# Performance work log

Measured on AMD Instinct MI355X. Metric: run time of the kernel, lower is better.

## Reference

```python
import jax, jax.numpy as jnp
import numpy as np

HS = WS = 1024      # downsampled mask dims (8192 / scale_factor 8)
K = 24              # kernel_num
KD = 35             # kernel_dim1 == kernel_dim2
OFF = HS // 2 - KD // 2  # offset_s = 495
MASK_STEEP = 4.0
MASK_SHIFT = 0.5
RESIST_STEEP = 50.0
RESIST_TH = 0.225
MAX_DOSE = 1.02
MIN_DOSE = 0.98
POOL = 3            # avepool_kernel


def setup_inputs() -> dict:
    key = jax.random.key(0)
    ks = jax.random.split(key, 7)
    return {
        "mask_s": jax.random.uniform(ks[0], (1, 1, HS, WS), dtype=jnp.float32),
        "kf_re": jax.random.normal(ks[1], (K, KD, KD), dtype=jnp.float32),
        "kf_im": jax.random.normal(ks[2], (K, KD, KD), dtype=jnp.float32),
        "kd_re": jax.random.normal(ks[3], (K, KD, KD), dtype=jnp.float32),
        "kd_im": jax.random.normal(ks[4], (K, KD, KD), dtype=jnp.float32),
        "kf_scale": jax.random.uniform(ks[5], (K, 1, 1), dtype=jnp.float32),
        "kd_scale": jax.random.uniform(ks[6], (K, 1, 1), dtype=jnp.float32),
    }


def _avgpool3(x):
    # AvgPool2d(kernel=3, stride=1, pad=1), count_include_pad=True -> always /9
    s = jax.lax.reduce_window(x, 0.0, jax.lax.add, (1, 1, POOL, POOL),
                              (1, 1, 1, 1),
                              [(0, 0), (0, 0), (POOL // 2, POOL // 2), (POOL // 2, POOL // 2)])
    return s / float(POOL * POOL)


def _dose_branch(crop, kernel, scale, dose):
    # crop: [1,1,KD,KD] complex ; kernel: [K,KD,KD] complex ; scale: [K,1,1]
    buf = jnp.zeros((1, K, HS, WS), dtype=jnp.complex64)
    buf = buf.at[:, :, OFF:OFF + KD, OFF:OFF + KD].set(crop * dose * kernel)
    img = jnp.fft.ifft2(buf)                      # [1,K,HS,WS] complex
    inten = (img.real * img.real + img.imag * img.imag) * scale
    inten = jnp.sum(inten, axis=1, keepdims=True)  # [1,1,HS,WS]
    return jax.nn.sigmoid(RESIST_STEEP * (inten - RESIST_TH))


def reference(mask_s, kf_re, kf_im, kd_re, kd_im, kf_scale, kd_scale):
    kf = jax.lax.complex(kf_re, kf_im)
    kd = jax.lax.complex(kd_re, kd_im)
    mask = jax.nn.sigmoid(MASK_STEEP * (_avgpool3(mask_s) - MASK_SHIFT))
    mf = jnp.fft.fftshift(jnp.fft.fft2(mask), axes=(-2, -1))  # [1,1,HS,WS]
    crop = mf[:, :, OFF:OFF + KD, OFF:OFF + KD]               # [1,1,KD,KD]
    x_nom = _dose_branch(crop, kf, kf_scale, 1.0)
    x_max = _dose_branch(crop, kf, kf_scale, MAX_DOSE)
    x_min = _dose_branch(crop, kd, kd_scale, MIN_DOSE)
    return x_nom, x_max, x_min
```

## Files before the change

### kernel.cpp

```cpp
#include <hip/hip_runtime.h>
#include <math.h>

#define HS 1024
#define WS 1024
#define KK 24
#define KD 35
#define NF 35
#define NDP 69
#define NTUP (2*KK*NDP)
#define CROW 40
#define PROW 37

#define G_OFF    0u
#define CROP_OFF 286720u
#define D_OFF    296520u
#define ZERO_QWORDS 6055

__global__ __launch_bounds__(256) void k_maskG(const float* __restrict__ ms,
                                               float2* __restrict__ G,
                                               unsigned long long* __restrict__ zq) {
    __shared__ float cs[WS + 2];
    __shared__ float m[WS];
    __shared__ float2 part[252];
    const int x = blockIdx.x;
    const int t = threadIdx.x;

    if (x < 24) {
        int i = x * 256 + t;
        if (i < ZERO_QWORDS) zq[i] = 0ull;
    }
    for (int j = t; j < WS; j += 256) {
        float a = (x > 0)      ? ms[(x - 1) * WS + j] : 0.0f;
        float b =                ms[x * WS + j];
        float d = (x < HS - 1) ? ms[(x + 1) * WS + j] : 0.0f;
        cs[j + 1] = a + b + d;
    }
    if (t == 0) { cs[0] = 0.0f; cs[WS + 1] = 0.0f; }
    __syncthreads();
    for (int j = t; j < WS; j += 256) {
        float pool = (cs[j] + cs[j + 1] + cs[j + 2]) * (1.0f / 9.0f);
        m[j] = 1.0f / (1.0f + expf(-4.0f * (pool - 0.5f)));
    }
    __syncthreads();
    if (t < 252) {
        const int qi = t / 14, seg = t % 14;
        float si, ci, ss, cc;
        sincospif(-(float)(qi * seg) * (1.0f / 512.0f), &si, &ci);
        sincospif(-(float)(qi * 14)  * (1.0f / 512.0f), &ss, &cc);
        float wr = ci, wi = si;
        float re = 0.0f, im = 0.0f;
        for (int y = seg; y < WS; y += 14) {
            float mv = m[y];
            re += mv * wr;
            im += mv * wi;
            float nr = wr * cc - wi * ss;
            wi = wr * ss + wi * cc;
            wr = nr;
        }
        part[t] = make_float2(re, im);
    }
    __syncthreads();
    if (t < 18) {
        float re = 0.0f, im = 0.0f;
        for (int s = 0; s < 14; ++s) { float2 p = part[t * 14 + s]; re += p.x; im += p.y; }
        G[(17 + t) * HS + x] = make_float2(re, im);
        if (t > 0) G[(17 - t) * HS + x] = make_float2(re, -im);
    }
}

__global__ __launch_bounds__(256) void k_crop(const float2* __restrict__ G,
                                              float2* __restrict__ crop) {
    __shared__ float2 g2[128];
    __shared__ float2 part[245];
    const int q  = blockIdx.x >> 3;
    const int xs = (blockIdx.x & 7) * 128;
    const int t  = threadIdx.x;
    if (t < 128) g2[t] = G[q * HS + xs + t];
    __syncthreads();
    if (t < 245) {
        const int p = t / 7, seg = t % 7;
        const int v = p - 17;
        float si, ci, ss, cc;
        sincospif((float)(v * (xs + seg)) * (1.0f / 512.0f), &si, &ci);
        sincospif((float)(v * 7)          * (1.0f / 512.0f), &ss, &cc);
        float wr = ci, wi = si;
        float re = 0.0f, im = 0.0f;
        for (int r = seg; r < 128; r += 7) {
            float2 gv = g2[r];
            re += gv.x * wr + gv.y * wi;
            im += gv.y * wr - gv.x * wi;
            float nr = wr * cc - wi * ss;
            wi = wr * ss + wi * cc;
            wr = nr;
        }
        part[t] = make_float2(re, im);
    }
    __syncthreads();
    if (t < NF) {
        float re = 0.0f, im = 0.0f;
        for (int s = 0; s < 7; ++s) { float2 p2 = part[t * 7 + s]; re += p2.x; im += p2.y; }
        float* dst = (float*)&crop[t * NF + q];
        atomicAdd(dst,     re);
        atomicAdd(dst + 1, im);
    }
}

__global__ __launch_bounds__(256) void k_D(
    const float2* __restrict__ crop,
    const float* __restrict__ kre0, const float* __restrict__ kim0,
    const float* __restrict__ kre1, const float* __restrict__ kim1,
    const float* __restrict__ sc0,  const float* __restrict__ sc1,
    float2* __restrict__ D)
{
    __shared__ float2 C[KD * CROW];
    __shared__ float2 partR[28 * PROW];
    const int tup = blockIdx.x;
    const int t   = threadIdx.x;

    const int b   = tup / (KK * NDP);
    const int rem = tup % (KK * NDP);
    const int k   = rem / NDP;
    const int idp = rem % NDP;
    const int dp  = idp - 34;
    const float* kre = b ? kre1 : kre0;
    const float* kim = b ? kim1 : kim0;
    const float dosefac = (b ? 0.98f : 1.0f) * (1.0f / 1048576.0f);
    const float sk2 = ((b ? sc1 : sc0)[k]) * dosefac * dosefac;

    if (t < 175) C[(t / 5) * CROW + 35 + (t % 5)] = make_float2(0.0f, 0.0f);
    #pragma unroll
    for (int j = 0; j < 5; ++j) {
        int i = t + j * 256;
        if (i < KD * KD) {
            float2 c = crop[i];
            int row = i / 35, col = i % 35;
            float kr = kre[k * KD * KD + i], ki = kim[k * KD * KD + i];
            C[row * CROW + col] = make_float2(c.x * kr - c.y * ki,
                                              c.x * ki + c.y * kr);
        }
    }
    __syncthreads();
    if (t < 252) {
        const int tile = t / 28;
        const int r    = t % 28;
        const int pgrp = r / 7;
        const int seg  = r % 7;
        const int d0   = tile * 4;
        const int plo = max(0, dp), phi = min(34, 34 + dp);
        float2 ac0 = {0,0}, ac1 = {0,0}, ac2 = {0,0}, ac3 = {0,0};
        for (int p = plo + pgrp; p <= phi; p += 4) {
            const float2* rowa = &C[p * CROW + d0];
            const float2* rowb = &C[(p - dp) * CROW];
            for (int u = seg; u <= 34 - d0; u += 7) {
                float2 bb = rowb[u];
                float2 a0 = rowa[u], a1 = rowa[u + 1], a2 = rowa[u + 2], a3 = rowa[u + 3];
                ac0.x += a0.x * bb.x + a0.y * bb.y;  ac0.y += a0.y * bb.x - a0.x * bb.y;
                ac1.x += a1.x * bb.x + a1.y * bb.y;  ac1.y += a1.y * bb.x - a1.x * bb.y;
                ac2.x += a2.x * bb.x + a2.y * bb.y;  ac2.y += a2.y * bb.x - a2.x * bb.y;
                ac3.x += a3.x * bb.x + a3.y * bb.y;  ac3.y += a3.y * bb.x - a3.x * bb.y;
            }
        }
        const int base = r * PROW + tile * 4;
        partR[base]     = ac0;
        partR[base + 1] = ac1;
        partR[base + 2] = ac2;
        partR[base + 3] = ac3;
    }
    __syncthreads();
    if (t < NF) {
        float re = 0.0f, im = 0.0f;
        for (int r = 0; r < 28; ++r) {
            float2 v = partR[r * PROW + t];
            re += v.x; im += v.y;
        }
        float* dst = (float*)&D[(b * NDP + idp) * NF + t];
        atomicAdd(dst,     re * sk2);
        atomicAdd(dst + 1, im * sk2);
    }
}

__global__ __launch_bounds__(256) void k_final(const float2* __restrict__ D,
                                               float* __restrict__ out) {
    __shared__ float2 partB[210];
    __shared__ float2 B[2][NF];
    const int x = blockIdx.x;
    const int t = threadIdx.x;
    if (t < 210) {
        const int s = t / 70, r = t % 70, b = r / 35, dq = r % 35;
        float si, ci, ss, cc;
        sincospif((float)((23 * s - 34) * x) * (1.0f / 512.0f), &si, &ci);
        sincospif((float)x                   * (1.0f / 512.0f), &ss, &cc);
        float wr = ci, wi = si;
        float re = 0.0f, im = 0.0f;
        const int i0 = 23 * s;
        for (int idp = i0; idp < i0 + 23; ++idp) {
            float2 d = D[(b * NDP + idp) * NF + dq];
            re += d.x * wr - d.y * wi;
            im += d.x * wi + d.y * wr;
            float nr = wr * cc - wi * ss;
            wi = wr * ss + wi * cc;
            wr = nr;
        }
        partB[t] = make_float2(re, im);
    }
    __syncthreads();
    if (t < 70) {
        float2 a = partB[t], b2 = partB[t + 70], c = partB[t + 140];
        B[t / 35][t % 35] = make_float2(a.x + b2.x + c.x, a.y + b2.y + c.y);
    }
    __syncthreads();
    const float bf0 = B[0][0].x;
    const float bd0 = B[1][0].x;
    for (int y = t; y < WS; y += 256) {
        float s1, c1;
        sincospif((float)y * (1.0f / 512.0f), &s1, &c1);
        float curx = c1, cury = s1;
        float sf = 0.0f, sd = 0.0f;
        #pragma unroll
        for (int dq = 1; dq < NF; ++dq) {
            float2 bf = B[0][dq], bd2 = B[1][dq];
            sf += bf.x * curx - bf.y * cury;
            sd += bd2.x * curx - bd2.y * cury;
            float nx = curx * c1 - cury * s1;
            cury = curx * s1 + cury * c1;
            curx = nx;
        }
        float If = bf0 + 2.0f * sf;
        float Id = bd0 + 2.0f * sd;
        int o = x * WS + y;
        out[o]               = 1.0f / (1.0f + expf(-50.0f * (If - 0.225f)));
        out[o + HS * WS]     = 1.0f / (1.0f + expf(-50.0f * (1.0404f * If - 0.225f)));
        out[o + 2 * HS * WS] = 1.0f / (1.0f + expf(-50.0f * (Id - 0.225f)));
    }
}

extern "C" void kernel_launch(void* const* d_in, const int* in_sizes, int n_in,
                              void* d_out, int out_size, void* d_ws, size_t ws_size,
                              hipStream_t stream) {
    (void)in_sizes; (void)n_in; (void)out_size; (void)ws_size;
    const float* ms    = (const float*)d_in[0];
    const float* kf_re = (const float*)d_in[1];
    const float* kf_im = (const float*)d_in[2];
    const float* kd_re = (const float*)d_in[3];
    const float* kd_im = (const float*)d_in[4];
    const float* kf_sc = (const float*)d_in[5];
    const float* kd_sc = (const float*)d_in[6];

    char* ws = (char*)d_ws;
    float2* G      = (float2*)(ws + G_OFF);
    float2* crop   = (float2*)(ws + CROP_OFF);
    float2* D      = (float2*)(ws + D_OFF);
    unsigned long long* zq = (unsigned long long*)(ws + CROP_OFF);
    float* out     = (float*)d_out;

    k_maskG<<<HS, 256, 0, stream>>>(ms, G, zq);
    k_crop<<<NF * 8, 256, 0, stream>>>(G, crop);
    k_D<<<NTUP, 256, 0, stream>>>(crop, kf_re, kf_im, kd_re, kd_im, kf_sc, kd_sc, D);
    k_final<<<HS, 256, 0, stream>>>(D, out);
}
```

Measured before the change: 58.76 us.

## Vectorize pooling loads, register-tile correlation inner loop, and write outputs as float4

The mask pooling stage now has each thread load and store four contiguous floats with float4 accesses instead of strided scalar loops. The correlation kernel gives each thread a contiguous 5-element u segment, which it unrolls with a sliding register window so A loads are reused, and the C row pad grows to 42. The final output stage computes four adjacent columns per thread and stores float4 vectors to all three outputs. The aim is fewer memory transactions and LDS loads, at the cost of more live registers per thread.

Result: slower. 61.61 us (+4.9%).

```diff
diff --git a/kernel.cpp b/kernel.cpp
--- a/kernel.cpp
+++ b/kernel.cpp
@@ -8,7 +8,7 @@
 #define NF 35
 #define NDP 69
 #define NTUP (2*KK*NDP)
-#define CROW 40
+#define CROW 42
 #define PROW 37
 
 #define G_OFF    0u
@@ -19,7 +19,7 @@
 __global__ __launch_bounds__(256) void k_maskG(const float* __restrict__ ms,
                                                float2* __restrict__ G,
                                                unsigned long long* __restrict__ zq) {
-    __shared__ float cs[WS + 2];
+    __shared__ float cs[WS + 8];
     __shared__ float m[WS];
     __shared__ float2 part[252];
     const int x = blockIdx.x;
@@ -29,17 +29,37 @@
         int i = x * 256 + t;
         if (i < ZERO_QWORDS) zq[i] = 0ull;
     }
-    for (int j = t; j < WS; j += 256) {
-        float a = (x > 0)      ? ms[(x - 1) * WS + j] : 0.0f;
-        float b =                ms[x * WS + j];
-        float d = (x < HS - 1) ? ms[(x + 1) * WS + j] : 0.0f;
-        cs[j + 1] = a + b + d;
-    }
-    if (t == 0) { cs[0] = 0.0f; cs[WS + 1] = 0.0f; }
-    __syncthreads();
-    for (int j = t; j < WS; j += 256) {
-        float pool = (cs[j] + cs[j + 1] + cs[j + 2]) * (1.0f / 9.0f);
-        m[j] = 1.0f / (1.0f + expf(-4.0f * (pool - 0.5f)));
+    {
+        const int j = 4 * t;
+        float4 b = *(const float4*)&ms[x * WS + j];
+        float4 a = make_float4(0.f, 0.f, 0.f, 0.f);
+        float4 d = make_float4(0.f, 0.f, 0.f, 0.f);
+        if (x > 0)      a = *(const float4*)&ms[(x - 1) * WS + j];
+        if (x < HS - 1) d = *(const float4*)&ms[(x + 1) * WS + j];
+        float4 s;
+        s.x = a.x + b.x + d.x;
+        s.y = a.y + b.y + d.y;
+        s.z = a.z + b.z + d.z;
+        s.w = a.w + b.w + d.w;
+        *(float4*)&cs[4 + j] = s;
+        if (t == 0) { cs[3] = 0.0f; cs[4 + WS] = 0.0f; }
+    }
+    __syncthreads();
+    {
+        const int j = 4 * t;
+        float4 c = *(const float4*)&cs[4 + j];
+        float l = cs[3 + j];
+        float r = cs[8 + j];
+        float p0 = (l   + c.x + c.y) * (1.0f / 9.0f);
+        float p1 = (c.x + c.y + c.z) * (1.0f / 9.0f);
+        float p2 = (c.y + c.z + c.w) * (1.0f / 9.0f);
+        float p3 = (c.z + c.w + r  ) * (1.0f / 9.0f);
+        float4 mv;
+        mv.x = 1.0f / (1.0f + expf(-4.0f * (p0 - 0.5f)));
+        mv.y = 1.0f / (1.0f + expf(-4.0f * (p1 - 0.5f)));
+        mv.z = 1.0f / (1.0f + expf(-4.0f * (p2 - 0.5f)));
+        mv.w = 1.0f / (1.0f + expf(-4.0f * (p3 - 0.5f)));
+        *(float4*)&m[j] = mv;
     }
     __syncthreads();
     if (t < 252) {
@@ -127,7 +147,7 @@
     const float dosefac = (b ? 0.98f : 1.0f) * (1.0f / 1048576.0f);
     const float sk2 = ((b ? sc1 : sc0)[k]) * dosefac * dosefac;
 
-    if (t < 175) C[(t / 5) * CROW + 35 + (t % 5)] = make_float2(0.0f, 0.0f);
+    if (t < 245) C[(t / 7) * CROW + 35 + (t % 7)] = make_float2(0.0f, 0.0f);
     #pragma unroll
     for (int j = 0; j < 5; ++j) {
         int i = t + j * 256;
@@ -144,20 +164,26 @@
         const int tile = t / 28;
         const int r    = t % 28;
         const int pgrp = r / 7;
-        const int seg  = r % 7;
+        const int useg = r % 7;
         const int d0   = tile * 4;
+        const int u0   = useg * 5;
         const int plo = max(0, dp), phi = min(34, 34 + dp);
         float2 ac0 = {0,0}, ac1 = {0,0}, ac2 = {0,0}, ac3 = {0,0};
-        for (int p = plo + pgrp; p <= phi; p += 4) {
-            const float2* rowa = &C[p * CROW + d0];
-            const float2* rowb = &C[(p - dp) * CROW];
-            for (int u = seg; u <= 34 - d0; u += 7) {
-                float2 bb = rowb[u];
-                float2 a0 = rowa[u], a1 = rowa[u + 1], a2 = rowa[u + 2], a3 = rowa[u + 3];
-                ac0.x += a0.x * bb.x + a0.y * bb.y;  ac0.y += a0.y * bb.x - a0.x * bb.y;
-                ac1.x += a1.x * bb.x + a1.y * bb.y;  ac1.y += a1.y * bb.x - a1.x * bb.y;
-                ac2.x += a2.x * bb.x + a2.y * bb.y;  ac2.y += a2.y * bb.x - a2.x * bb.y;
-                ac3.x += a3.x * bb.x + a3.y * bb.y;  ac3.y += a3.y * bb.x - a3.x * bb.y;
+        if (u0 <= 34 - d0) {
+            for (int p = plo + pgrp; p <= phi; p += 4) {
+                const float2* rowa = &C[p * CROW + d0 + u0];
+                const float2* rowb = &C[(p - dp) * CROW + u0];
+                float2 a0 = rowa[0], a1 = rowa[1], a2 = rowa[2];
+                #pragma unroll
+                for (int s = 0; s < 5; ++s) {
+                    float2 a3 = rowa[s + 3];
+                    float2 bb = rowb[s];
+                    ac0.x += a0.x * bb.x + a0.y * bb.y;  ac0.y += a0.y * bb.x - a0.x * bb.y;
+                    ac1.x += a1.x * bb.x + a1.y * bb.y;  ac1.y += a1.y * bb.x - a1.x * bb.y;
+                    ac2.x += a2.x * bb.x + a2.y * bb.y;  ac2.y += a2.y * bb.x - a2.x * bb.y;
+                    ac3.x += a3.x * bb.x + a3.y * bb.y;  ac3.y += a3.y * bb.x - a3.x * bb.y;
+                    a0 = a1; a1 = a2; a2 = a3;
+                }
             }
         }
         const int base = r * PROW + tile * 4;
@@ -211,27 +237,40 @@
     __syncthreads();
     const float bf0 = B[0][0].x;
     const float bd0 = B[1][0].x;
-    for (int y = t; y < WS; y += 256) {
-        float s1, c1;
-        sincospif((float)y * (1.0f / 512.0f), &s1, &c1);
-        float curx = c1, cury = s1;
-        float sf = 0.0f, sd = 0.0f;
+    const int y0 = t * 4;
+    float c1[4], s1[4], cx[4], cy[4], sf[4], sd[4];
+    #pragma unroll
+    for (int j = 0; j < 4; ++j) {
+        sincospif((float)(y0 + j) * (1.0f / 512.0f), &s1[j], &c1[j]);
+        cx[j] = c1[j]; cy[j] = s1[j];
+        sf[j] = 0.0f;  sd[j] = 0.0f;
+    }
+    #pragma unroll
+    for (int dq = 1; dq < NF; ++dq) {
+        const float2 bf  = B[0][dq];
+        const float2 bd2 = B[1][dq];
         #pragma unroll
-        for (int dq = 1; dq < NF; ++dq) {
-            float2 bf = B[0][dq], bd2 = B[1][dq];
-            sf += bf.x * curx - bf.y * cury;
-            sd += bd2.x * curx - bd2.y * cury;
-            float nx = curx * c1 - cury * s1;
-            cury = curx * s1 + cury * c1;
-            curx = nx;
-        }
-        float If = bf0 + 2.0f * sf;
-        float Id = bd0 + 2.0f * sd;
-        int o = x * WS + y;
-        out[o]               = 1.0f / (1.0f + expf(-50.0f * (If - 0.225f)));
-        out[o + HS * WS]     = 1.0f / (1.0f + expf(-50.0f * (1.0404f * If - 0.225f)));
-        out[o + 2 * HS * WS] = 1.0f / (1.0f + expf(-50.0f * (Id - 0.225f)));
-    }
+        for (int j = 0; j < 4; ++j) {
+            sf[j] += bf.x * cx[j] - bf.y * cy[j];
+            sd[j] += bd2.x * cx[j] - bd2.y * cy[j];
+            float nx = cx[j] * c1[j] - cy[j] * s1[j];
+            cy[j] = cx[j] * s1[j] + cy[j] * c1[j];
+            cx[j] = nx;
+        }
+    }
+    float r0[4], r1[4], r2[4];
+    #pragma unroll
+    for (int j = 0; j < 4; ++j) {
+        float If = bf0 + 2.0f * sf[j];
+        float Id = bd0 + 2.0f * sd[j];
+        r0[j] = 1.0f / (1.0f + expf(-50.0f * (If - 0.225f)));
+        r1[j] = 1.0f / (1.0f + expf(-50.0f * (1.0404f * If - 0.225f)));
+        r2[j] = 1.0f / (1.0f + expf(-50.0f * (Id - 0.225f)));
+    }
+    const int o = x * WS + y0;
+    *(float4*)&out[o]               = make_float4(r0[0], r0[1], r0[2], r0[3]);
+    *(float4*)&out[o + HS * WS]     = make_float4(r1[0], r1[1], r1[2], r1[3]);
+    *(float4*)&out[o + 2 * HS * WS] = make_float4(r2[0], r2[1], r2[2], r2[3]);
 }
 
 extern "C" void kernel_launch(void* const* d_in, const int* in_sizes, int n_in,
```
